# Performance work log

Hardware: AMD Instinct MI355X
Metric: run time of the kernel (lower is better)

Reference implementation:

```python
import jax, jax.numpy as jnp
import numpy as np

E, D, H = 8, 1024, 4096  # num_experts, backbone hidden, moe hidden
B, S = 4, 4096
TEMPERATURE = 1.0


def setup_inputs() -> dict:
    key = jax.random.key(0)
    ks = jax.random.split(key, 7)
    sc = 0.02
    return {
        "x": jax.random.normal(ks[0], (B, S, D), dtype=jnp.float32),
        "W1": jax.random.normal(ks[1], (E, D, H), dtype=jnp.float32) * sc,
        "b1": jax.random.normal(ks[2], (E, H), dtype=jnp.float32) * sc,
        "W2": jax.random.normal(ks[3], (E, H, D), dtype=jnp.float32) * sc,
        "b2": jax.random.normal(ks[4], (E, D), dtype=jnp.float32) * sc,
        "Wr": jax.random.normal(ks[5], (D, E), dtype=jnp.float32) * sc,
        "br": jax.random.normal(ks[6], (E,), dtype=jnp.float32) * sc,
    }


def reference(x, W1, b1, W2, b2, Wr, br):
    # Router: logits -> temperature -> softmax -> top-1 expert index per token
    routing_logits = (x @ Wr + br) / TEMPERATURE          # [B,S,E]
    routing_probs = jax.nn.softmax(routing_logits, axis=-1)
    indices = jnp.argmax(routing_probs, axis=-1)          # [B,S] (top-1)

    # Faithful to source: every expert runs on the masked (zeroed) inputs,
    # so each expert's bias path expert_i(0) is added for every token.
    out = jnp.zeros_like(x)
    num_experts = W1.shape[0]
    for i in range(num_experts):  # fixed small loop over experts
        mask = (indices == i).astype(x.dtype)[..., None]  # [B,S,1]
        xi = x * mask                                     # [B,S,D]
        h = jax.nn.relu(xi @ W1[i] + b1[i])               # [B,S,H]
        out = out + (h @ W2[i] + b2[i])                   # [B,S,D]
    return out
```

## Files before the change

### kernel.cpp

```cpp
#include <hip/hip_runtime.h>
#include <cstdint>

#define E_ 8
#define D_ 1024
#define H_ 4096
#define NTOK 16384

typedef unsigned short ushort_t;
typedef __attribute__((ext_vector_type(8))) short short8;
typedef __attribute__((ext_vector_type(4))) float f32x4;

__device__ __forceinline__ ushort_t f2bf(float f) {
  uint32_t u = __builtin_bit_cast(uint32_t, f);
  uint32_t r = (u + 0x7fffu + ((u >> 16) & 1u)) >> 16;
  return (ushort_t)r;
}

__device__ __forceinline__ void gload_lds16(const void* g, void* l) {
  __builtin_amdgcn_global_load_lds(
      (const __attribute__((address_space(1))) uint32_t*)g,
      (__attribute__((address_space(3))) uint32_t*)l, 16, 0, 0);
}

__global__ void init_kernel(float* rawbase) {
  int tid = threadIdx.x + blockIdx.x * 256;
  if (tid < E_ * D_) rawbase[tid] = 0.f;
}

template <int FUSE>
__global__ void transpose_bf16(const float* __restrict__ in, ushort_t* __restrict__ out,
                               int R, int C, const float* __restrict__ b1,
                               float* __restrict__ rawbase) {
  __shared__ ushort_t t[64][70];
  __shared__ float scs[16][64];
  __shared__ float relu_b1[64];
  const int e = blockIdx.z;
  const float* ip = in + (size_t)e * R * C;
  ushort_t* op = out + (size_t)e * R * C;
  const int c0 = blockIdx.x * 64, r0 = blockIdx.y * 64;
  const int tid = threadIdx.x;
  if (FUSE) {
    if (tid < 64) relu_b1[tid] = fmaxf(b1[e * R + r0 + tid], 0.f);
    __syncthreads();
  }
  const int rsub = tid >> 4;
  const int c4 = (tid & 15) * 4;
  float s0 = 0.f, s1 = 0.f, s2 = 0.f, s3 = 0.f;
#pragma unroll
  for (int q = 0; q < 4; ++q) {
    int r = q * 16 + rsub;
    float4 v = *(const float4*)&ip[(size_t)(r0 + r) * C + c0 + c4];
    t[c4 + 0][r] = f2bf(v.x);
    t[c4 + 1][r] = f2bf(v.y);
    t[c4 + 2][r] = f2bf(v.z);
    t[c4 + 3][r] = f2bf(v.w);
    if (FUSE) {
      float rb = relu_b1[r];
      s0 += rb * v.x; s1 += rb * v.y; s2 += rb * v.z; s3 += rb * v.w;
    }
  }
  if (FUSE) {
    scs[rsub][c4 + 0] = s0; scs[rsub][c4 + 1] = s1;
    scs[rsub][c4 + 2] = s2; scs[rsub][c4 + 3] = s3;
  }
  __syncthreads();
  if (FUSE && tid < 64) {
    float tot = 0.f;
#pragma unroll
    for (int g = 0; g < 16; ++g) tot += scs[g][tid];
    atomicAdd(&rawbase[e * D_ + c0 + tid], tot);
  }
#pragma unroll
  for (int it = 0; it < 2; ++it) {
    int idx = it * 256 + tid;
    int c = idx >> 3, g = idx & 7;
    short8 v;
#pragma unroll
    for (int k = 0; k < 8; ++k) v[k] = (short)t[c][g * 8 + k];
    *(short8*)&op[(size_t)(c0 + c) * R + r0 + g * 8] = v;
  }
}

__global__ void adj_kernel(const float* __restrict__ rawbase, const float* __restrict__ b2,
                           float* __restrict__ adj) {
  int i = blockIdx.x * 256 + threadIdx.x;
  int d = i & (D_ - 1);
  int e = i >> 10;
  float tot = 0.f;
#pragma unroll
  for (int ii = 0; ii < E_; ++ii) tot += rawbase[ii * D_ + d] + b2[ii * D_ + d];
  adj[i] = tot - rawbase[e * D_ + d];
}

__global__ void router_convert(const float* __restrict__ x, const float* __restrict__ Wr,
                               const float* __restrict__ br, int* __restrict__ idx,
                               ushort_t* __restrict__ xb) {
  __shared__ float wr_s[E_][D_];
  const int tid = threadIdx.x;
  for (int j = tid; j < E_ * D_; j += 256) {
    int e = j & 7, d = j >> 3;
    wr_s[e][d] = Wr[j];
  }
  __syncthreads();
  const int wid = tid >> 6, l = tid & 63;
  const int t0 = blockIdx.x * 32 + wid * 8;
  for (int tt = 0; tt < 8; ++tt) {
    int t = t0 + tt;
    const float4* xr4 = (const float4*)(x + (size_t)t * D_);
    ushort4* xo4 = (ushort4*)(xb + (size_t)t * D_);
    float s[E_];
#pragma unroll
    for (int e = 0; e < E_; ++e) s[e] = 0.f;
#pragma unroll
    for (int q = 0; q < 4; ++q) {
      float4 xv = xr4[q * 64 + l];
      ushort4 o;
      o.x = f2bf(xv.x); o.y = f2bf(xv.y); o.z = f2bf(xv.z); o.w = f2bf(xv.w);
      xo4[q * 64 + l] = o;
#pragma unroll
      for (int e = 0; e < E_; ++e) {
        const float4 wv = *(const float4*)&wr_s[e][(q * 64 + l) * 4];
        s[e] += xv.x * wv.x + xv.y * wv.y + xv.z * wv.z + xv.w * wv.w;
      }
    }
#pragma unroll
    for (int e = 0; e < E_; ++e) {
#pragma unroll
      for (int off = 32; off > 0; off >>= 1) s[e] += __shfl_xor(s[e], off, 64);
    }
    if (l == 0) {
      float best = s[0] + br[0];
      int bi = 0;
#pragma unroll
      for (int e = 1; e < E_; ++e) {
        float v = s[e] + br[e];
        if (v > best) { best = v; bi = e; }
      }
      idx[t] = bi;
    }
  }
}

__global__ void count_scan_build(const int* __restrict__ idx, int* __restrict__ offsets,
                                 int* __restrict__ work1, int* __restrict__ work2,
                                 int* __restrict__ meta, int* __restrict__ perm) {
  __shared__ int hist[256][E_];
  __shared__ int pb[256][E_];
  __shared__ int esum[E_];
  __shared__ int nt[E_], b1s[E_ + 1], b2s[E_ + 1];
  __shared__ int offs_s[E_];
  const int tid = threadIdx.x;
  int c[E_];
#pragma unroll
  for (int e = 0; e < E_; ++e) c[e] = 0;
  for (int t = tid; t < NTOK; t += 256) ++c[idx[t]];
#pragma unroll
  for (int e = 0; e < E_; ++e) hist[tid][e] = c[e];
  __syncthreads();
  {
    const int hw = tid >> 5, l32 = tid & 31;
    int carry = 0;
#pragma unroll
    for (int ch = 0; ch < 8; ++ch) {
      int v = hist[ch * 32 + l32][hw];
      int s = v;
#pragma unroll
      for (int off = 1; off < 32; off <<= 1) {
        int t = __shfl_up(s, off, 32);
        if (l32 >= off) s += t;
      }
      pb[ch * 32 + l32][hw] = carry + s - v;
      carry += __shfl(s, 31, 32);
    }
    if (l32 == 0) esum[hw] = carry;
  }
  __syncthreads();
  if (tid == 0) {
    int acc = 0, w1 = 0, w2 = 0;
    for (int e = 0; e < E_; ++e) {
      int s = esum[e];
      offsets[e] = acc;
      offs_s[e] = acc;
      acc += s;
      int n = (s + 255) >> 8;
      nt[e] = n;
      b1s[e] = w1; w1 += n * (H_ / 256);
      b2s[e] = w2; w2 += n * (D_ / 256);
    }
    offsets[E_] = acc;
    b1s[E_] = w1;
    b2s[E_] = w2;
    meta[0] = w1;
    meta[1] = w2;
  }
  __syncthreads();
  for (int t = tid; t < NTOK; t += 256) {
    int e = idx[t];
    int p = pb[tid][e]++;
    perm[offs_s[e] + p] = t;
  }
  if (tid < E_) {
    const int e = tid, n = nt[e];
    int p = b1s[e];
    for (int tmg = 0; tmg < n; tmg += 4) {
      int tmh = (tmg + 4 < n) ? (tmg + 4) : n;
      for (int tn = 0; tn < H_ / 256; ++tn)
        for (int tm = tmg; tm < tmh; ++tm)
          work1[p++] = (e << 16) | (tm << 8) | tn;
    }
  } else if (tid < 2 * E_) {
    const int e = tid - E_, n = nt[e];
    int p = b2s[e];
    for (int tmg = 0; tmg < n; tmg += 4) {
      int tmh = (tmg + 4 < n) ? (tmg + 4) : n;
      for (int tn = 0; tn < D_ / 256; ++tn)
        for (int tm = tmg; tm < tmh; ++tm)
          work2[p++] = (e << 16) | (tm << 8) | tn;
    }
  }
}


template <int MODE>
__global__ __launch_bounds__(512, 2) void ffn_gemm(
    const ushort_t* __restrict__ A_all, const ushort_t* __restrict__ Bw,
    const float* __restrict__ bias, const int* __restrict__ offs,
    const int* __restrict__ perm, float* __restrict__ out, ushort_t* __restrict__ hbo,
    const int* __restrict__ work, const int* __restrict__ nw_p) {
  constexpr int KdF = (MODE == 1) ? D_ : H_;
  constexpr int Nd = (MODE == 1) ? H_ : D_;
  constexpr int NKT = KdF / 32;

  const int n1 = *nw_p;
  int bid = blockIdx.x;
  if (bid >= n1) return;
  {
    int q = n1 >> 3, r = n1 & 7;
    int xcd = bid & 7, pos = bid >> 3;
    bid = (xcd < r ? xcd * (q + 1) : r * (q + 1) + (xcd - r) * q) + pos;
  }
  const int item = work[bid];
  const int e = (item >> 16) & 255, tm = (item >> 8) & 255, tn = item & 255;
  const int ms = offs[e];
  const int M = offs[e + 1] - ms;

  __shared__ __align__(16) ushort_t lds[4][2][8192];

  const int tid = threadIdx.x;
  const int wid = tid >> 6, l = tid & 63;
  const int wm = wid >> 2, wn = wid & 3;
  const int lr = l & 15, lh = l >> 4;

  const ushort_t* Bb = Bw + (size_t)e * ((size_t)Nd * KdF);
  const int arow0 = tm * 256;
  const int brow0 = tn * 256;
  const int rowmaxA = M - 1;

  size_t a_src[2];
  int b_src[2];
#pragma unroll
  for (int c = 0; c < 2; ++c) {
    int s = c * 512 + tid;
    int P = s >> 3, U = s & 7;
    int Ur = U ^ (P & 7);
    int r = 2 * P + (Ur >> 2);
    int u = Ur & 3;
    int ga = arow0 + r;
    if (ga > rowmaxA) ga = rowmaxA;
    int arow = (MODE == 1) ? perm[ms + ga] : (ms + ga);
    a_src[c] = (size_t)arow * KdF + u * 8;
    b_src[c] = (brow0 + r) * KdF + u * 8;
  }

#define STAGE(buf, kt)                                                                   \
  _Pragma("unroll") for (int c_ = 0; c_ < 2; ++c_) {                                     \
    gload_lds16(A_all + a_src[c_] + (kt) * 32, &lds[buf][0][(c_ * 512 + wid * 64) * 8]); \
    gload_lds16(Bb + b_src[c_] + (kt) * 32, &lds[buf][1][(c_ * 512 + wid * 64) * 8]);    \
  }

#define AOFF(r) (((((r) >> 1)) << 6) + ((((lh) + (((r) & 1) << 2)) ^ (((r) >> 1) & 7)) << 3))

  f32x4 acc[8][4];
#pragma unroll
  for (int i = 0; i < 8; ++i)
#pragma unroll
    for (int j = 0; j < 4; ++j) acc[i][j] = (f32x4){0.f, 0.f, 0.f, 0.f};

  STAGE(0, 0)
  STAGE(1, 1)
  STAGE(2, 2)
  asm volatile("s_waitcnt vmcnt(8)" ::: "memory");
  __builtin_amdgcn_s_barrier();

#pragma unroll 4
  for (int kt = 0; kt < NKT; ++kt) {
    int pf = kt + 3;
    if (pf > NKT - 1) pf = NKT - 1;
    STAGE((kt + 3) & 3, pf)
    const ushort_t* la = &lds[kt & 3][0][0];
    const ushort_t* lb = &lds[kt & 3][1][0];
    short8 af[8], bq[4];
#pragma unroll
    for (int i = 0; i < 8; ++i)
      af[i] = *(const short8*)&la[AOFF(wm * 128 + i * 16 + lr)];
#pragma unroll
    for (int j = 0; j < 4; ++j)
      bq[j] = *(const short8*)&lb[AOFF(wn * 64 + j * 16 + lr)];
#pragma unroll
    for (int i = 0; i < 8; ++i)
#pragma unroll
      for (int j = 0; j < 4; ++j)
        acc[i][j] = __builtin_amdgcn_mfma_f32_16x16x32_bf16(af[i], bq[j], acc[i][j], 0, 0, 0);
    asm volatile("s_waitcnt vmcnt(8)" ::: "memory");
    __builtin_amdgcn_s_barrier();
  }

  const int gcolbase = tn * 256 + wn * 64 + lr;
  float bv[4];
#pragma unroll
  for (int j = 0; j < 4; ++j) bv[j] = bias[e * Nd + gcolbase + j * 16];
#pragma unroll
  for (int i = 0; i < 8; ++i) {
#pragma unroll
    for (int rr = 0; rr < 4; ++rr) {
      int grow = tm * 256 + wm * 128 + i * 16 + lh * 4 + rr;
      if (grow < M) {
        if (MODE == 1) {
          size_t rowoff = (size_t)(ms + grow) * H_;
#pragma unroll
          for (int j = 0; j < 4; ++j) {
            float v = acc[i][j][rr] + bv[j];
            v = fmaxf(v, 0.f);
            hbo[rowoff + gcolbase + j * 16] = f2bf(v);
          }
        } else {
          int tok = perm[ms + grow];
          size_t rowoff = (size_t)tok * D_;
#pragma unroll
          for (int j = 0; j < 4; ++j)
            out[rowoff + gcolbase + j * 16] = acc[i][j][rr] + bv[j];
        }
      }
    }
  }
#undef STAGE
#undef AOFF
}

extern "C" void kernel_launch(void* const* d_in, const int* in_sizes, int n_in,
                              void* d_out, int out_size, void* d_ws, size_t ws_size,
                              hipStream_t stream) {
  const float* x  = (const float*)d_in[0];
  const float* W1 = (const float*)d_in[1];
  const float* b1 = (const float*)d_in[2];
  const float* W2 = (const float*)d_in[3];
  const float* b2 = (const float*)d_in[4];
  const float* Wr = (const float*)d_in[5];
  const float* br = (const float*)d_in[6];
  float* out = (float*)d_out;

  char* ws = (char*)d_ws;
  ushort_t* W1t   = (ushort_t*)(ws);
  ushort_t* W2t   = (ushort_t*)(ws + 67108864);
  ushort_t* xb    = (ushort_t*)(ws + 134217728);
  ushort_t* hb    = (ushort_t*)(ws + 167772160);
  float*    rawbase = (float*)(ws + 301989888);
  float*    adj   = (float*)(ws + 302022656);
  int*      idx   = (int*)(ws + 302055424);
  int*      perm  = (int*)(ws + 302120960);
  int*      offsets = (int*)(ws + 302186624);
  int*      meta   = (int*)(ws + 302186752);
  int*      work1  = (int*)(ws + 302186880);
  int*      work2  = (int*)(ws + 302195072);

  init_kernel<<<32, 256, 0, stream>>>(rawbase);
  transpose_bf16<0><<<dim3(H_ / 64, D_ / 64, E_), 256, 0, stream>>>(W1, W1t, D_, H_,
                                                                    nullptr, nullptr);
  transpose_bf16<1><<<dim3(D_ / 64, H_ / 64, E_), 256, 0, stream>>>(W2, W2t, H_, D_,
                                                                    b1, rawbase);
  adj_kernel<<<32, 256, 0, stream>>>(rawbase, b2, adj);
  router_convert<<<512, 256, 0, stream>>>(x, Wr, br, idx, xb);
  count_scan_build<<<1, 256, 0, stream>>>(idx, offsets, work1, work2, meta, perm);
  ffn_gemm<1><<<1136, 512, 0, stream>>>(xb, W1t, b1, offsets, perm, nullptr, hb,
                                        work1, meta + 0);
  ffn_gemm<2><<<284, 512, 0, stream>>>(hb, W2t, adj, offsets, perm, out, nullptr,
                                       work2, meta + 1);
}
```

Before: 588.5 us.

## Deepen GEMM LDS ring to five stages, two k-tiles per barrier

Grows the shared-memory staging ring from four to five buffers and restructures the main k-loop to process two 32-wide k-tiles per iteration. Each iteration issues two prefetches and two MFMA compute phases, with only one vmcnt wait and workgroup barrier. The aim is to halve barrier and wait overhead per k-tile and keep more loads in flight. The cost is the full 160KB LDS budget and non-power-of-two buffer indexing with runtime modulo arithmetic, which could reduce unrolling and scheduling quality.

```diff
diff --git a/kernel.cpp b/kernel.cpp
--- a/kernel.cpp
+++ b/kernel.cpp
@@ -244,7 +244,7 @@
   const int ms = offs[e];
   const int M = offs[e + 1] - ms;
 
-  __shared__ __align__(16) ushort_t lds[4][2][8192];
+  __shared__ __align__(16) ushort_t lds[5][2][8192];
 
   const int tid = threadIdx.x;
   const int wid = tid >> 6, l = tid & 63;
@@ -280,6 +280,21 @@
 
 #define AOFF(r) (((((r) >> 1)) << 6) + ((((lh) + (((r) & 1) << 2)) ^ (((r) >> 1) & 7)) << 3))
 
+#define COMPUTE(buf)                                                                     \
+  {                                                                                      \
+    const ushort_t* la = &lds[buf][0][0];                                                \
+    const ushort_t* lb = &lds[buf][1][0];                                                \
+    short8 af[8], bq[4];                                                                 \
+    _Pragma("unroll") for (int i = 0; i < 8; ++i)                                        \
+      af[i] = *(const short8*)&la[AOFF(wm * 128 + i * 16 + lr)];                         \
+    _Pragma("unroll") for (int j = 0; j < 4; ++j)                                        \
+      bq[j] = *(const short8*)&lb[AOFF(wn * 64 + j * 16 + lr)];                          \
+    _Pragma("unroll") for (int i = 0; i < 8; ++i)                                        \
+      _Pragma("unroll") for (int j = 0; j < 4; ++j)                                      \
+        acc[i][j] = __builtin_amdgcn_mfma_f32_16x16x32_bf16(af[i], bq[j], acc[i][j],     \
+                                                            0, 0, 0);                    \
+  }
+
   f32x4 acc[8][4];
 #pragma unroll
   for (int i = 0; i < 8; ++i)
@@ -289,30 +304,23 @@
   STAGE(0, 0)
   STAGE(1, 1)
   STAGE(2, 2)
-  asm volatile("s_waitcnt vmcnt(8)" ::: "memory");
+  asm volatile("s_waitcnt vmcnt(4)" ::: "memory");
   __builtin_amdgcn_s_barrier();
 
-#pragma unroll 4
-  for (int kt = 0; kt < NKT; ++kt) {
-    int pf = kt + 3;
-    if (pf > NKT - 1) pf = NKT - 1;
-    STAGE((kt + 3) & 3, pf)
-    const ushort_t* la = &lds[kt & 3][0][0];
-    const ushort_t* lb = &lds[kt & 3][1][0];
-    short8 af[8], bq[4];
-#pragma unroll
-    for (int i = 0; i < 8; ++i)
-      af[i] = *(const short8*)&la[AOFF(wm * 128 + i * 16 + lr)];
-#pragma unroll
-    for (int j = 0; j < 4; ++j)
-      bq[j] = *(const short8*)&lb[AOFF(wn * 64 + j * 16 + lr)];
-#pragma unroll
-    for (int i = 0; i < 8; ++i)
-#pragma unroll
-      for (int j = 0; j < 4; ++j)
-        acc[i][j] = __builtin_amdgcn_mfma_f32_16x16x32_bf16(af[i], bq[j], acc[i][j], 0, 0, 0);
-    asm volatile("s_waitcnt vmcnt(8)" ::: "memory");
+  int bw = 0;
+  for (int w = 0; w < NKT; w += 2) {
+    int pf0 = w + 3; if (pf0 > NKT - 1) pf0 = NKT - 1;
+    int pf1 = w + 4; if (pf1 > NKT - 1) pf1 = NKT - 1;
+    int s0 = bw + 3; if (s0 >= 5) s0 -= 5;
+    int s1 = bw + 4; if (s1 >= 5) s1 -= 5;
+    int b1x = bw + 1; if (b1x >= 5) b1x -= 5;
+    STAGE(s0, pf0)
+    COMPUTE(bw)
+    STAGE(s1, pf1)
+    COMPUTE(b1x)
+    asm volatile("s_waitcnt vmcnt(4)" ::: "memory");
     __builtin_amdgcn_s_barrier();
+    bw += 2; if (bw >= 5) bw -= 5;
   }
 
   const int gcolbase = tn * 256 + wn * 64 + lr;
@@ -345,6 +353,7 @@
   }
 #undef STAGE
 #undef AOFF
+#undef COMPUTE
 }
 
 extern "C" void kernel_launch(void* const* d_in, const int* in_sizes, int n_in,
```

Measured after the change: 589.1 us. Within noise of the previous version (+0.1%).
